# Kernel tuning notes

Measured on AMD Instinct MI355X. Metric: run time of the kernel, lower is better.

Reference implementation:

```python
import jax, jax.numpy as jnp
import numpy as np

N = 1024          # number of junctions
H = 1024          # heatmap height
W = 1024          # heatmap width
NUM_SAMPLES = 64  # samples along each candidate segment (torch_sampler)
DETECT_THRESH = 0.5
INLIER_THRESH = 0.99


def setup_inputs() -> dict:
    key = jax.random.key(0)
    k1, k2 = jax.random.split(key)
    # junctions are (h, w) float coordinates inside the image
    junctions = jax.random.uniform(k1, (N, 2), dtype=jnp.float32) * (H - 1)
    heatmap = jax.random.uniform(k2, (H, W), dtype=jnp.float32)
    return {"junctions": junctions, "heatmap": heatmap}


def _bilinear_sample(heatmap, ch, cw):
    """SOLD2 detect_bilinear: gather 4 corners, bilinear weights. ch/cw: [N,N,S]."""
    hf = jnp.floor(ch); hc = jnp.ceil(ch)
    wf = jnp.floor(cw); wc = jnp.ceil(cw)
    hfi = hf.astype(jnp.int32); hci = hc.astype(jnp.int32)
    wfi = wf.astype(jnp.int32); wci = wc.astype(jnp.int32)
    return (heatmap[hfi, wfi] * (hc - ch) * (wc - cw)
          + heatmap[hfi, wci] * (hc - ch) * (cw - wf)
          + heatmap[hci, wfi] * (ch - hf) * (wc - cw)
          + heatmap[hci, wci] * (ch - hf) * (cw - wf))


def reference(junctions, heatmap):
    n = junctions.shape[0]
    Hh, Ww = heatmap.shape
    t = jnp.linspace(0.0, 1.0, NUM_SAMPLES, dtype=jnp.float32)  # [S]
    # cand_samples[i, j, s] = junc[i] * t[s] + junc[j] * (1 - t[s])  (start=i, end=j)
    ch = junctions[:, None, 0:1] * t + junctions[None, :, 0:1] * (1.0 - t)  # [N,N,S]
    cw = junctions[:, None, 1:2] * t + junctions[None, :, 1:2] * (1.0 - t)  # [N,N,S]
    ch = jnp.clip(ch, 0.0, Hh - 1)
    cw = jnp.clip(cw, 0.0, Ww - 1)
    feat = _bilinear_sample(heatmap, ch, cw)                    # [N,N,S]
    mean_feat = feat.mean(axis=-1)                              # [N,N]
    inlier_ratio = (feat > DETECT_THRESH).astype(jnp.float32).mean(axis=-1)
    # candidate map: strict upper triangle (torch.triu(ones, diagonal=1))
    cand_mask = jnp.triu(jnp.ones((n, n), dtype=bool), k=1)
    detected = (mean_feat > DETECT_THRESH) & (inlier_ratio >= INLIER_THRESH) & cand_mask
    line_map = (detected | detected.T).astype(jnp.int32)        # symmetric line map
    return line_map, mean_feat
```

## Files before the change

kernel.cpp:

```cpp
#include <hip/hip_runtime.h>

#define NJ 1024
#define DETECT 0.5f
#define RESCUE 0.4975f

__device__ __forceinline__ float sample_t(int s) {
    return (s == 63) ? 1.0f : (float)s * (1.0f / 63.0f);
}

__device__ __forceinline__ int tiled_idx(int h, int w) {
    return ((h >> 2) << 12) + ((w >> 2) << 4) + ((h & 3) << 2) + (w & 3);
}

__device__ __forceinline__ void exact_pair(const float2 ja, const float2 jb,
                                           const float* __restrict__ heat,
                                           float& mean_o, float& min_o)
{
    float acc = 0.0f;
    float mn  = __builtin_inff();
    for (int s = 0; s < 64; ++s) {
        const float t  = sample_t(s);
        const float om = 1.0f - t;
        float ch = __fadd_rn(__fmul_rn(ja.x, t), __fmul_rn(jb.x, om));
        float cw = __fadd_rn(__fmul_rn(ja.y, t), __fmul_rn(jb.y, om));
        ch = fminf(fmaxf(ch, 0.0f), 1023.0f);
        cw = fminf(fmaxf(cw, 0.0f), 1023.0f);
        const float hf = floorf(ch), hc = ceilf(ch);
        const float wf = floorf(cw), wc = ceilf(cw);
        const int hfi = (int)hf, hci = (int)hc;
        const int wfi = (int)wf, wci = (int)wc;
        const float a00 = heat[(hfi << 10) + wfi];
        const float a01 = heat[(hfi << 10) + wci];
        const float a10 = heat[(hci << 10) + wfi];
        const float a11 = heat[(hci << 10) + wci];
        const float t1 = __fmul_rn(__fmul_rn(a00, __fsub_rn(hc, ch)), __fsub_rn(wc, cw));
        const float t2 = __fmul_rn(__fmul_rn(a01, __fsub_rn(hc, ch)), __fsub_rn(cw, wf));
        const float t3 = __fmul_rn(__fmul_rn(a10, __fsub_rn(ch, hf)), __fsub_rn(wc, cw));
        const float t4 = __fmul_rn(__fmul_rn(a11, __fsub_rn(ch, hf)), __fsub_rn(cw, wf));
        const float feat = __fadd_rn(__fadd_rn(__fadd_rn(t1, t2), t3), t4);
        acc += feat;
        mn = fminf(mn, feat);
    }
    mean_o = acc * (1.0f / 64.0f);
    min_o  = mn;
}

__device__ __forceinline__ unsigned int expand_bits16(unsigned int v) {
    v &= 0x0000FFFFu;
    v = (v | (v << 8)) & 0x00FF00FFu;
    v = (v | (v << 4)) & 0x0F0F0F0Fu;
    v = (v | (v << 2)) & 0x33333333u;
    v = (v | (v << 1)) & 0x55555555u;
    return v;
}

__global__ __launch_bounds__(256) void prep_kernel(
    const float* __restrict__ junc, const float* __restrict__ heat,
    unsigned int* __restrict__ packed, float2* __restrict__ sortedJ,
    int* __restrict__ perm, float* __restrict__ line_out,
    float* __restrict__ mean_out)
{
    const int b = blockIdx.x;
    if (b < 1024) {
        const int idx = b * 256 + threadIdx.x;
        const int h = idx >> 8;
        const int w4 = (idx & 255) << 2;
        const int hn = (h < 1023) ? h + 1 : 1023;
        const float* r0 = heat + (h  << 10);
        const float* r1 = heat + (hn << 10);
        const float4 a = *(const float4*)(r0 + w4);
        const float4 bq = *(const float4*)(r1 + w4);
        const int wnext = (w4 + 4 <= 1023) ? w4 + 4 : 1023;
        const float a4 = r0[wnext];
        const float b4 = r1[wnext];

        const float av[5] = {a.x, a.y, a.z, a.w, a4};
        const float bv[5] = {bq.x, bq.y, bq.z, bq.w, b4};
        unsigned int out[4];
        #pragma unroll
        for (int u = 0; u < 4; ++u) {
            const unsigned int c0 = (unsigned int)__float2int_rn(av[u]     * 255.0f);
            const unsigned int c1 = (unsigned int)__float2int_rn(av[u + 1] * 255.0f);
            const unsigned int c2 = (unsigned int)__float2int_rn(bv[u]     * 255.0f);
            const unsigned int c3 = (unsigned int)__float2int_rn(bv[u]     * 0.0f
                                   + bv[u + 1] * 255.0f);
            out[u] = c0 | (c1 << 8) | (c2 << 16) | (c3 << 24);
        }
        *(uint4*)(packed + tiled_idx(h, w4)) = make_uint4(out[0], out[1], out[2], out[3]);
    } else if (b == 1024) {
        __shared__ unsigned int   sk[1024];
        __shared__ unsigned short sv[1024];
        const int t = threadIdx.x;
        #pragma unroll
        for (int m = 0; m < 4; ++m) {
            const int i = (m << 8) + t;
            const float2 jc2 = ((const float2*)junc)[i];
            const int mh = min(max((int)jc2.x, 0), 1023);
            const int mw = min(max((int)jc2.y, 0), 1023);
            sk[i] = (expand_bits16((unsigned int)mh) << 1)
                  |  expand_bits16((unsigned int)mw);
            sv[i] = (unsigned short)i;
        }
        __syncthreads();
        for (unsigned int k = 2; k <= 1024; k <<= 1) {
            for (unsigned int s = k >> 1; s > 0; s >>= 1) {
                #pragma unroll
                for (int m = 0; m < 4; ++m) {
                    const int i = (m << 8) + t;
                    const int l = i ^ (int)s;
                    if (l > i) {
                        const unsigned int ka = sk[i], kb = sk[l];
                        const bool up = ((i & (int)k) == 0);
                        if ((ka > kb) == up) {
                            sk[i] = kb; sk[l] = ka;
                            const unsigned short va = sv[i];
                            sv[i] = sv[l]; sv[l] = va;
                        }
                    }
                }
                __syncthreads();
            }
        }
        #pragma unroll
        for (int m = 0; m < 4; ++m) {
            const int i = (m << 8) + t;
            const int src = (int)sv[i];
            perm[i] = src;
            sortedJ[i] = ((const float2*)junc)[src];
        }
    } else {
        const int i = ((b - 1025) << 8) + threadIdx.x;
        const float2 ji = ((const float2*)junc)[i];
        float mean, mn;
        exact_pair(ji, ji, heat, mean, mn);
        mean_out[(i << 10) + i] = mean;
        line_out[(i << 10) + i] = 0.0f;
    }
}

__global__ __launch_bounds__(256) void sold2_thread_kernel(
    const float2* __restrict__ sortedJ,
    const int* __restrict__ perm,
    const float* __restrict__ heat,
    const unsigned int* __restrict__ packed,
    float* __restrict__ line_out,
    float* __restrict__ mean_out)
{
    const int q = blockIdx.x * 256 + threadIdx.x;
    const int r = q >> 9;
    const int c = 1 + (q & 511);
    const int jc = (r + c) & 1023;

    const float2 jr = sortedJ[r];
    const float2 jj = sortedJ[jc];

    float acc = 0.0f;
    float mn  = __builtin_inff();

    #pragma unroll
    for (int s0 = 0; s0 < 64; s0 += 16) {
        float chv[16], cwv[16];
        unsigned int cv[16];
        #pragma unroll
        for (int u = 0; u < 16; ++u) {
            const int s = s0 + u;
            const float t  = sample_t(s);
            const float om = 1.0f - t;
            float ch = __fadd_rn(__fmul_rn(jr.x, t), __fmul_rn(jj.x, om));
            float cw = __fadd_rn(__fmul_rn(jr.y, t), __fmul_rn(jj.y, om));
            ch = fminf(fmaxf(ch, 0.0f), 1023.0f);
            cw = fminf(fmaxf(cw, 0.0f), 1023.0f);
            chv[u] = ch;
            cwv[u] = cw;
            const int hfi = (int)ch;
            const int wfi = (int)cw;
            cv[u] = packed[tiled_idx(hfi, wfi)];
        }
        #pragma unroll
        for (int u = 0; u < 16; ++u) {
            const float ch = chv[u], cw = cwv[u];
            const float hf = floorf(ch), hc = ceilf(ch);
            const float wf = floorf(cw), wc = ceilf(cw);
            const float wh0 = hc - ch, wh1 = ch - hf;
            const float ww0 = wc - cw, ww1 = cw - wf;
            const unsigned int cc = cv[u];
            const float a00 = (float)(cc & 0xffu);
            const float a01 = (float)((cc >> 8) & 0xffu);
            const float a10 = (float)((cc >> 16) & 0xffu);
            const float a11 = (float)(cc >> 24);
            const float feat = a00 * (wh0 * ww0) + a01 * (wh0 * ww1)
                             + a10 * (wh1 * ww0) + a11 * (wh1 * ww1);
            acc += feat;
            mn = fminf(mn, feat);
        }
    }

    float mean = acc * (1.0f / (255.0f * 64.0f));
    const float mns = mn * (1.0f / 255.0f);

    bool det = false;
    if ((mns > RESCUE) && (mean > RESCUE)) {
        float mn2;
        exact_pair(jr, jj, heat, mean, mn2);
        det = (mean > DETECT) && (mn2 > DETECT);
    }

    const int io = perm[r];
    const int jo = perm[jc];
    const float lv = det ? 1.0f : 0.0f;

    const int p1 = (io << 10) + jo;
    __builtin_nontemporal_store(mean, mean_out + p1);
    __builtin_nontemporal_store(lv,   line_out + p1);

    if (c != 512) {
        const int p2 = (jo << 10) + io;
        __builtin_nontemporal_store(mean, mean_out + p2);
        __builtin_nontemporal_store(lv,   line_out + p2);
    }
}

extern "C" void kernel_launch(void* const* d_in, const int* in_sizes, int n_in,
                              void* d_out, int out_size, void* d_ws, size_t ws_size,
                              hipStream_t stream) {
    const float* junc = (const float*)d_in[0];
    const float* heat = (const float*)d_in[1];
    float* line_out = (float*)d_out;
    float* mean_out = line_out + NJ * NJ;

    unsigned int* packed = (unsigned int*)d_ws;
    float2* sortedJ = (float2*)((char*)d_ws + (4u << 20));
    int* perm = (int*)((char*)d_ws + (4u << 20) + 8192);

    prep_kernel<<<1029, 256, 0, stream>>>(junc, heat, packed, sortedJ, perm,
                                          line_out, mean_out);

    const int total = NJ * 512;
    sold2_thread_kernel<<<total / 256, 256, 0, stream>>>(sortedJ, perm, heat,
                                                         packed, line_out, mean_out);
}
```

Before: 186.7 us.

## Pack heatmap in 4x4 tiles per thread, rank-sort junctions, fold diagonal into main kernel

The prep kernel now has each thread quantize a 5x5 neighbourhood and write a whole 4x4 packed tile, which cuts redundant heatmap reads and the number of blocks from 1024 to 256. The bitonic sort is replaced with a counting-rank sort over Morton keys that have the index appended so every key is unique. The separate diagonal blocks are removed and the main kernel covers 513 columns per row, so the c=0 case writes the diagonal directly. In exchange the main kernel now does an integer division by 513, and the diagonal mean comes from the quantized approximation instead of the exact path.

```diff
diff --git a/kernel.cpp b/kernel.cpp
--- a/kernel.cpp
+++ b/kernel.cpp
@@ -57,84 +57,75 @@
 __global__ __launch_bounds__(256) void prep_kernel(
     const float* __restrict__ junc, const float* __restrict__ heat,
     unsigned int* __restrict__ packed, float2* __restrict__ sortedJ,
-    int* __restrict__ perm, float* __restrict__ line_out,
-    float* __restrict__ mean_out)
+    int* __restrict__ perm)
 {
     const int b = blockIdx.x;
-    if (b < 1024) {
-        const int idx = b * 256 + threadIdx.x;
-        const int h = idx >> 8;
-        const int w4 = (idx & 255) << 2;
-        const int hn = (h < 1023) ? h + 1 : 1023;
-        const float* r0 = heat + (h  << 10);
-        const float* r1 = heat + (hn << 10);
-        const float4 a = *(const float4*)(r0 + w4);
-        const float4 bq = *(const float4*)(r1 + w4);
-        const int wnext = (w4 + 4 <= 1023) ? w4 + 4 : 1023;
-        const float a4 = r0[wnext];
-        const float b4 = r1[wnext];
-
-        const float av[5] = {a.x, a.y, a.z, a.w, a4};
-        const float bv[5] = {bq.x, bq.y, bq.z, bq.w, b4};
-        unsigned int out[4];
-        #pragma unroll
-        for (int u = 0; u < 4; ++u) {
-            const unsigned int c0 = (unsigned int)__float2int_rn(av[u]     * 255.0f);
-            const unsigned int c1 = (unsigned int)__float2int_rn(av[u + 1] * 255.0f);
-            const unsigned int c2 = (unsigned int)__float2int_rn(bv[u]     * 255.0f);
-            const unsigned int c3 = (unsigned int)__float2int_rn(bv[u]     * 0.0f
-                                   + bv[u + 1] * 255.0f);
-            out[u] = c0 | (c1 << 8) | (c2 << 16) | (c3 << 24);
-        }
-        *(uint4*)(packed + tiled_idx(h, w4)) = make_uint4(out[0], out[1], out[2], out[3]);
-    } else if (b == 1024) {
-        __shared__ unsigned int   sk[1024];
-        __shared__ unsigned short sv[1024];
+    if (b < 256) {
+        const int idx = (b << 8) + threadIdx.x;
+        const int th = idx >> 8;
+        const int tw = idx & 255;
+        const int h0 = th << 2;
+        const int w0 = tw << 2;
+
+        float v[5][5];
+        #pragma unroll
+        for (int a = 0; a < 5; ++a) {
+            const int h = (h0 + a <= 1023) ? h0 + a : 1023;
+            const float* row = heat + (h << 10);
+            const float4 f4 = *(const float4*)(row + w0);
+            v[a][0] = f4.x; v[a][1] = f4.y; v[a][2] = f4.z; v[a][3] = f4.w;
+            const int w4 = (w0 + 4 <= 1023) ? w0 + 4 : 1023;
+            v[a][4] = row[w4];
+        }
+
+        unsigned int q[5][5];
+        #pragma unroll
+        for (int a = 0; a < 5; ++a)
+            #pragma unroll
+            for (int c = 0; c < 5; ++c)
+                q[a][c] = (unsigned int)__float2int_rn(v[a][c] * 255.0f);
+
+        unsigned int out[16];
+        #pragma unroll
+        for (int a = 0; a < 4; ++a)
+            #pragma unroll
+            for (int c = 0; c < 4; ++c)
+                out[(a << 2) + c] = q[a][c] | (q[a][c + 1] << 8)
+                                  | (q[a + 1][c] << 16) | (q[a + 1][c + 1] << 24);
+
+        uint4* dst = (uint4*)(packed + ((th << 12) + (tw << 4)));
+        dst[0] = make_uint4(out[0],  out[1],  out[2],  out[3]);
+        dst[1] = make_uint4(out[4],  out[5],  out[6],  out[7]);
+        dst[2] = make_uint4(out[8],  out[9],  out[10], out[11]);
+        dst[3] = make_uint4(out[12], out[13], out[14], out[15]);
+    } else {
+        __shared__ unsigned int keys[1024];
         const int t = threadIdx.x;
+        unsigned int mykey[4];
         #pragma unroll
         for (int m = 0; m < 4; ++m) {
             const int i = (m << 8) + t;
             const float2 jc2 = ((const float2*)junc)[i];
             const int mh = min(max((int)jc2.x, 0), 1023);
             const int mw = min(max((int)jc2.y, 0), 1023);
-            sk[i] = (expand_bits16((unsigned int)mh) << 1)
-                  |  expand_bits16((unsigned int)mw);
-            sv[i] = (unsigned short)i;
+            const unsigned int mort = (expand_bits16((unsigned int)mh) << 1)
+                                    |  expand_bits16((unsigned int)mw);
+            mykey[m] = (mort << 10) | (unsigned int)i;
+            keys[i] = mykey[m];
         }
         __syncthreads();
-        for (unsigned int k = 2; k <= 1024; k <<= 1) {
-            for (unsigned int s = k >> 1; s > 0; s >>= 1) {
-                #pragma unroll
-                for (int m = 0; m < 4; ++m) {
-                    const int i = (m << 8) + t;
-                    const int l = i ^ (int)s;
-                    if (l > i) {
-                        const unsigned int ka = sk[i], kb = sk[l];
-                        const bool up = ((i & (int)k) == 0);
-                        if ((ka > kb) == up) {
-                            sk[i] = kb; sk[l] = ka;
-                            const unsigned short va = sv[i];
-                            sv[i] = sv[l]; sv[l] = va;
-                        }
-                    }
-                }
-                __syncthreads();
-            }
+        int rank[4] = {0, 0, 0, 0};
+        for (int k = 0; k < 1024; ++k) {
+            const unsigned int kk = keys[k];
+            #pragma unroll
+            for (int m = 0; m < 4; ++m) rank[m] += (kk < mykey[m]) ? 1 : 0;
         }
         #pragma unroll
         for (int m = 0; m < 4; ++m) {
             const int i = (m << 8) + t;
-            const int src = (int)sv[i];
-            perm[i] = src;
-            sortedJ[i] = ((const float2*)junc)[src];
-        }
-    } else {
-        const int i = ((b - 1025) << 8) + threadIdx.x;
-        const float2 ji = ((const float2*)junc)[i];
-        float mean, mn;
-        exact_pair(ji, ji, heat, mean, mn);
-        mean_out[(i << 10) + i] = mean;
-        line_out[(i << 10) + i] = 0.0f;
+            perm[rank[m]] = i;
+            sortedJ[rank[m]] = ((const float2*)junc)[i];
+        }
     }
 }
 
@@ -147,8 +138,8 @@
     float* __restrict__ mean_out)
 {
     const int q = blockIdx.x * 256 + threadIdx.x;
-    const int r = q >> 9;
-    const int c = 1 + (q & 511);
+    const int r = q / 513;
+    const int c = q - r * 513;
     const int jc = (r + c) & 1023;
 
     const float2 jr = sortedJ[r];
@@ -199,7 +190,7 @@
     const float mns = mn * (1.0f / 255.0f);
 
     bool det = false;
-    if ((mns > RESCUE) && (mean > RESCUE)) {
+    if ((mns > RESCUE) && (mean > RESCUE) && (c != 0)) {
         float mn2;
         exact_pair(jr, jj, heat, mean, mn2);
         det = (mean > DETECT) && (mn2 > DETECT);
@@ -213,7 +204,7 @@
     __builtin_nontemporal_store(mean, mean_out + p1);
     __builtin_nontemporal_store(lv,   line_out + p1);
 
-    if (c != 512) {
+    if (c != 0 && c != 512) {
         const int p2 = (jo << 10) + io;
         __builtin_nontemporal_store(mean, mean_out + p2);
         __builtin_nontemporal_store(lv,   line_out + p2);
@@ -232,10 +223,9 @@
     float2* sortedJ = (float2*)((char*)d_ws + (4u << 20));
     int* perm = (int*)((char*)d_ws + (4u << 20) + 8192);
 
-    prep_kernel<<<1029, 256, 0, stream>>>(junc, heat, packed, sortedJ, perm,
-                                          line_out, mean_out);
-
-    const int total = NJ * 512;
+    prep_kernel<<<257, 256, 0, stream>>>(junc, heat, packed, sortedJ, perm);
+
+    const int total = NJ * 513;
     sold2_thread_kernel<<<total / 256, 256, 0, stream>>>(sortedJ, perm, heat,
                                                          packed, line_out, mean_out);
 }
```

Measured after the change: 185.6 us. No clear change (-0.6%).
